# Kernel tuning notes

Measured on AMD Instinct MI355X. Metric: run time of the kernel, lower is better.

Reference implementation:

```python
import jax, jax.numpy as jnp
import numpy as np

B, N, DX, DZ, L = 512, 32, 78, 64, 1000

def _gcn_norm(A):
    # PyG gcn_norm: add remaining self loops (fill 1), symmetric D^-1/2 (A+I) D^-1/2
    n = A.shape[-1]
    A_hat = jnp.maximum(A, jnp.eye(n, dtype=A.dtype))
    dinv = jax.lax.rsqrt(A_hat.sum(-1))
    return A_hat * dinv[..., :, None] * dinv[..., None, :]

def _bn(h, g, b, eps=1e-5):
    # BatchNorm1d, training-mode batch statistics (torch default module state)
    m = jnp.mean(h, 0)
    v = jnp.var(h, 0)
    return (h - m) * jax.lax.rsqrt(v + eps) * g + b

def _conv(h, W, b):  # h [B,C,L], W [O,I,K], valid padding + ReLU (Conv1dReLU)
    y = jax.lax.conv_general_dilated(h, W, (1,), 'VALID', dimension_numbers=('NCH', 'OIH', 'NCH'))
    return jax.nn.relu(y + b[None, :, None])

def _attn(v):  # Attention.project is only Tanh in the source
    return jax.nn.softmax(jnp.tanh(v), axis=1) * v

def _forward(x, adj, target, z, dec_W0, dec_b0, dec_g0, dec_be0, dec_W1, dec_b1, dec_g1, dec_be1,
             gW1, gb1, gW2, gb2, gW3, gb3, fcg1_W, fcg1_b, fcg2_W, fcg2_b, emb,
             c10_W, c10_b, c20_W, c20_b, c21_W, c21_b, c30_W, c30_b, c31_W, c31_b, c32_W, c32_b,
             prot_W, prot_b, fc1_W, fc1_b, fc2_W, fc2_b, out_W, out_b):
    Bn = B * N
    # frozen conditional VAE decoder -> augmented features (detached)
    zc = jnp.concatenate([z.reshape(Bn, DZ), x.reshape(Bn, DX)], axis=-1)
    h = jax.nn.relu(_bn(zc @ dec_W0 + dec_b0, dec_g0, dec_be0))
    aug = jnp.tanh(_bn(h @ dec_W1 + dec_b1, dec_g1, dec_be1))
    aug = jax.lax.stop_gradient(aug).reshape(B, N, DX)
    X = jnp.concatenate([aug, x], axis=-1)  # [B,N,156]
    # 1-hop / 2-hop / 3-hop adjacency patterns (spspmm -> binary power patterns)
    A1 = _gcn_norm(adj)
    A2p = (adj @ adj > 0).astype(adj.dtype)
    A3p = (A2p @ adj > 0).astype(adj.dtype)
    A2 = _gcn_norm(A2p)
    A3 = _gcn_norm(A3p)
    gcn = lambda A, hh, W, b: jax.nn.relu(A @ (hh @ W) + b)
    h1 = gcn(A1, X, gW1, gb1)
    h2 = gcn(A1, h1, gW2, gb2)
    h3 = gcn(A1, h2, gW3, gb3)
    h5 = gcn(A2, gcn(A2, X, gW1, gb1), gW2, gb2)
    h6 = gcn(A3, X, gW1, gb1)
    hg = jnp.max(jnp.concatenate([h3, h5, h6], axis=-1), axis=1)  # gmp -> [B,1092]
    xg = jax.nn.relu(hg @ fcg1_W + fcg1_b) @ fcg2_W + fcg2_b  # dropout = identity (eval)
    xg = _attn(xg)
    # protein branch
    e = jnp.transpose(emb[target], (0, 2, 1))  # [B,128,1000]
    f1 = jnp.max(_conv(e, c10_W, c10_b), axis=-1)
    f2 = jnp.max(_conv(_conv(e, c20_W, c20_b), c21_W, c21_b), axis=-1)
    f3 = jnp.max(_conv(_conv(_conv(e, c30_W, c30_b), c31_W, c31_b), c32_W, c32_b), axis=-1)
    xt = _attn(jnp.concatenate([f1, f2, f3], axis=-1) @ prot_W + prot_b)
    xc = jnp.concatenate([xg, xt], axis=-1)
    xc = jax.nn.relu(xc @ fc1_W + fc1_b)
    xc = jax.nn.relu(xc @ fc2_W + fc2_b)
    return xc @ out_W + out_b

def setup_inputs():
    key = jax.random.key(0)
    ks = iter(jax.random.split(key, 64))
    def w(shape, s=0.05):
        return jax.random.normal(next(ks), shape, dtype=jnp.float32) * s
    x = jax.random.normal(next(ks), (B, N, DX), dtype=jnp.float32)
    r = jax.random.uniform(next(ks), (B, N, N))
    up = jnp.triu((r < 0.08).astype(jnp.float32), 1)
    adj = up + jnp.swapaxes(up, 1, 2)  # symmetric, no self loops, avg degree ~5
    target = jax.random.randint(next(ks), (B, L), 0, 26, dtype=jnp.int32)
    z = jax.random.normal(next(ks), (B, N, DZ), dtype=jnp.float32)
    emb = w((26, 128), 1.0).at[0].set(0.0)  # padding_idx=0
    return dict(x=x, adj=adj, target=target, z=z,
        dec_W0=w((DZ + DX, 256)), dec_b0=jnp.zeros(256), dec_g0=jnp.ones(256), dec_be0=jnp.zeros(256),
        dec_W1=w((256, DX)), dec_b1=jnp.zeros(DX), dec_g1=jnp.ones(DX), dec_be1=jnp.zeros(DX),
        gW1=w((156, 156)), gb1=jnp.zeros(156), gW2=w((156, 312)), gb2=jnp.zeros(312),
        gW3=w((312, 624)), gb3=jnp.zeros(624),
        fcg1_W=w((1092, 1024)), fcg1_b=jnp.zeros(1024), fcg2_W=w((1024, 128)), fcg2_b=jnp.zeros(128),
        emb=emb,
        c10_W=w((96, 128, 3)), c10_b=jnp.zeros(96),
        c20_W=w((96, 128, 3)), c20_b=jnp.zeros(96), c21_W=w((96, 96, 3)), c21_b=jnp.zeros(96),
        c30_W=w((96, 128, 3)), c30_b=jnp.zeros(96), c31_W=w((96, 96, 3)), c31_b=jnp.zeros(96),
        c32_W=w((96, 96, 3)), c32_b=jnp.zeros(96),
        prot_W=w((288, 128)), prot_b=jnp.zeros(128),
        fc1_W=w((256, 1024)), fc1_b=jnp.zeros(1024), fc2_W=w((1024, 512)), fc2_b=jnp.zeros(512),
        out_W=w((512, 1)), out_b=jnp.zeros(1))

def reference(x, adj, target, z, dec_W0, dec_b0, dec_g0, dec_be0, dec_W1, dec_b1, dec_g1, dec_be1,
              gW1, gb1, gW2, gb2, gW3, gb3, fcg1_W, fcg1_b, fcg2_W, fcg2_b, emb,
              c10_W, c10_b, c20_W, c20_b, c21_W, c21_b, c30_W, c30_b, c31_W, c31_b, c32_W, c32_b,
              prot_W, prot_b, fc1_W, fc1_b, fc2_W, fc2_b, out_W, out_b):
    return _forward(x, adj, target, z, dec_W0, dec_b0, dec_g0, dec_be0, dec_W1, dec_b1, dec_g1, dec_be1,
                    gW1, gb1, gW2, gb2, gW3, gb3, fcg1_W, fcg1_b, fcg2_W, fcg2_b, emb,
                    c10_W, c10_b, c20_W, c20_b, c21_W, c21_b, c30_W, c30_b, c31_W, c31_b, c32_W, c32_b,
                    prot_W, prot_b, fc1_W, fc1_b, fc2_W, fc2_b, out_W, out_b)
```

## Files before the change

### kernel.cpp

```cpp
#include <hip/hip_runtime.h>

static constexpr size_t O_H0    = 0;
static constexpr size_t O_H1P   = 4194304;
static constexpr size_t O_X     = 5473216;
static constexpr size_t O_A1    = 8029120;
static constexpr size_t O_A2    = 8553408;
static constexpr size_t O_A3    = 9077696;
static constexpr size_t O_H4    = 9601984;
static constexpr size_t O_H6    = 12157888;
static constexpr size_t O_H1W2  = 14713792;
static constexpr size_t O_H2    = 19825600;
static constexpr size_t O_H2W3  = 24937408;
static constexpr size_t O_H3    = 35161024;
static constexpr size_t O_HG    = 45384640;
static constexpr size_t O_FCG1O = 45943744;
static constexpr size_t O_M     = 46468032;
static constexpr size_t O_F     = 46535424;
static constexpr size_t O_V     = 46682880;
static constexpr size_t O_XC    = 46748416;
static constexpr size_t O_FC1O  = 46879488;
static constexpr size_t O_FC2O  = 47403776;
static constexpr size_t O_PART  = 47665920;
static constexpr size_t O_MV    = 47698688;
static constexpr size_t O_BT21  = 47699712;
static constexpr size_t O_BT31  = 47727360;
static constexpr size_t O_W32T  = 47755008;
static constexpr size_t O_XW1  = O_H0;
static constexpr size_t O_SK   = O_H0;
static constexpr size_t O_H1   = O_X;
static constexpr size_t O_H4W2 = O_H1W2;
static constexpr size_t O_H5   = O_H2W3;
static constexpr size_t O_R10  = O_H1W2;
static constexpr size_t O_R20  = O_H1W2 + 1687296;
static constexpr size_t O_R30  = O_H1W2 + 3374592;
static constexpr size_t O_N21  = O_H2W3;
static constexpr size_t O_N31  = O_H2W3 + 5061888;

template<int AMODE, int ACT>
__global__ __launch_bounds__(256) void gemm_k(
    const float* __restrict__ A, const float* __restrict__ Bm,
    const float* __restrict__ bias, float* __restrict__ C,
    int M, int N, int K, const float* __restrict__ A2)
{
  __shared__ __align__(16) float sA[16 * 68];
  __shared__ __align__(16) float sB[16 * 68];
  const int tid = threadIdx.x;
  const int m0 = blockIdx.y * 64, n0 = blockIdx.x * 64;
  const int tx = tid & 15, ty = tid >> 4;
  float acc[4][4] = {};
  for (int k0 = 0; k0 < K; k0 += 16) {
#pragma unroll
    for (int s2 = 0; s2 < 4; s2++) {
      int idx = tid + s2 * 256;
      int am = idx >> 4, ak = idx & 15;
      int gm = m0 + am, gk = k0 + ak;
      float va = 0.f;
      if (gm < M && gk < K) {
        if (AMODE == 0) va = A[(size_t)gm * K + gk];
        else            va = (gk < 64) ? A[gm * 64 + gk] : A2[gm * 78 + gk - 64];
      }
      sA[ak * 68 + am] = va;
      int bk2 = idx >> 6, bn = idx & 63;
      int gk2 = k0 + bk2, gn = n0 + bn;
      float vb = 0.f;
      if (gk2 < K && gn < N) vb = Bm[(size_t)gk2 * N + gn];
      sB[bk2 * 68 + bn] = vb;
    }
    __syncthreads();
#pragma unroll
    for (int kk = 0; kk < 16; kk++) {
      const float4 a4 = *(const float4*)&sA[kk * 68 + ty * 4];
      const float4 b4 = *(const float4*)&sB[kk * 68 + tx * 4];
      const float ra[4] = {a4.x, a4.y, a4.z, a4.w};
      const float rb[4] = {b4.x, b4.y, b4.z, b4.w};
#pragma unroll
      for (int i2 = 0; i2 < 4; i2++)
#pragma unroll
        for (int j2 = 0; j2 < 4; j2++)
          acc[i2][j2] = fmaf(ra[i2], rb[j2], acc[i2][j2]);
    }
    __syncthreads();
  }
#pragma unroll
  for (int i2 = 0; i2 < 4; i2++) {
    int gm = m0 + ty * 4 + i2;
    if (gm >= M) continue;
#pragma unroll
    for (int j2 = 0; j2 < 4; j2++) {
      int gn = n0 + tx * 4 + j2;
      if (gn >= N) continue;
      float v = acc[i2][j2];
      if (bias) v += bias[gn];
      if (ACT == 1) v = fmaxf(v, 0.f);
      C[(size_t)gm * N + gn] = v;
    }
  }
}

__global__ __launch_bounds__(256) void gemm_sk(
    const float* __restrict__ A, const float* __restrict__ Bm,
    float* __restrict__ PT, int M, int N, int K, int KS)
{
  __shared__ __align__(16) float sA[16 * 68];
  __shared__ __align__(16) float sB[16 * 68];
  const int tid = threadIdx.x;
  const int m0 = blockIdx.y * 64, n0 = blockIdx.x * 64;
  const int kb = blockIdx.z * KS;
  const int ke = min(K, kb + KS);
  const int tx = tid & 15, ty = tid >> 4;
  float acc[4][4] = {};
  for (int k0 = kb; k0 < ke; k0 += 16) {
#pragma unroll
    for (int s2 = 0; s2 < 4; s2++) {
      int idx = tid + s2 * 256;
      int am = idx >> 4, ak = idx & 15;
      int gm = m0 + am, gk = k0 + ak;
      float va = 0.f;
      if (gm < M && gk < ke) va = A[(size_t)gm * K + gk];
      sA[ak * 68 + am] = va;
      int bk2 = idx >> 6, bn = idx & 63;
      int gk2 = k0 + bk2, gn = n0 + bn;
      float vb = 0.f;
      if (gk2 < ke && gn < N) vb = Bm[(size_t)gk2 * N + gn];
      sB[bk2 * 68 + bn] = vb;
    }
    __syncthreads();
#pragma unroll
    for (int kk = 0; kk < 16; kk++) {
      const float4 a4 = *(const float4*)&sA[kk * 68 + ty * 4];
      const float4 b4 = *(const float4*)&sB[kk * 68 + tx * 4];
      const float ra[4] = {a4.x, a4.y, a4.z, a4.w};
      const float rb[4] = {b4.x, b4.y, b4.z, b4.w};
#pragma unroll
      for (int i2 = 0; i2 < 4; i2++)
#pragma unroll
        for (int j2 = 0; j2 < 4; j2++)
          acc[i2][j2] = fmaf(ra[i2], rb[j2], acc[i2][j2]);
    }
    __syncthreads();
  }
  float* P = PT + (size_t)blockIdx.z * M * N;
#pragma unroll
  for (int i2 = 0; i2 < 4; i2++) {
    int gm = m0 + ty * 4 + i2;
    if (gm >= M) continue;
#pragma unroll
    for (int j2 = 0; j2 < 4; j2++) {
      int gn = n0 + tx * 4 + j2;
      if (gn >= N) continue;
      P[(size_t)gm * N + gn] = acc[i2][j2];
    }
  }
}

__global__ void skred_kernel(const float* __restrict__ PT, const float* __restrict__ bias,
                             float* __restrict__ C, int MN, int nmask, int S, int act)
{
  int i = blockIdx.x * 256 + threadIdx.x;
  if (i >= MN) return;
  float s = 0.f;
  for (int z = 0; z < S; z++) s += PT[(size_t)z * MN + i];
  if (bias) s += bias[i & nmask];
  if (act) s = fmaxf(s, 0.f);
  C[i] = s;
}

template<int AMODE, int ACT>
__global__ __launch_bounds__(256) void gemm2_k(
    const float* __restrict__ A, const float* __restrict__ Bm,
    const float* __restrict__ bias, float* __restrict__ C,
    int M, int N, int K, const float* __restrict__ A2)
{
  __shared__ __align__(16) float sA[16 * 132];
  __shared__ __align__(16) float sB[16 * 68];
  const int tid = threadIdx.x;
  const int m0 = blockIdx.y * 128, n0 = blockIdx.x * 64;
  const int tx = tid & 15, ty = tid >> 4;
  float acc[8][4] = {};
  for (int k0 = 0; k0 < K; k0 += 16) {
#pragma unroll
    for (int s2 = 0; s2 < 2; s2++) {
      int idx = tid + s2 * 256;
      int am = idx >> 2, kq = idx & 3;
      int gm = m0 + am;
#pragma unroll
      for (int j = 0; j < 4; j++) {
        int gk = k0 + kq * 4 + j;
        float va = 0.f;
        if (gm < M && gk < K) {
          if (AMODE == 0) va = A[(size_t)gm * K + gk];
          else            va = (gk < 64) ? A[gm * 64 + gk] : A2[gm * 78 + gk - 64];
        }
        sA[(kq * 4 + j) * 132 + am] = va;
      }
    }
    {
      int bk = tid >> 4, bn4 = tid & 15;
      int gk2 = k0 + bk;
#pragma unroll
      for (int j = 0; j < 4; j++) {
        int gn = n0 + bn4 * 4 + j;
        float vb = 0.f;
        if (gk2 < K && gn < N) vb = Bm[(size_t)gk2 * N + gn];
        sB[bk * 68 + bn4 * 4 + j] = vb;
      }
    }
    __syncthreads();
#pragma unroll
    for (int kk = 0; kk < 16; kk++) {
      const float4 a0 = *(const float4*)&sA[kk * 132 + ty * 8];
      const float4 a1 = *(const float4*)&sA[kk * 132 + ty * 8 + 4];
      const float4 b4 = *(const float4*)&sB[kk * 68 + tx * 4];
      const float ra[8] = {a0.x, a0.y, a0.z, a0.w, a1.x, a1.y, a1.z, a1.w};
      const float rb[4] = {b4.x, b4.y, b4.z, b4.w};
#pragma unroll
      for (int i2 = 0; i2 < 8; i2++)
#pragma unroll
        for (int j2 = 0; j2 < 4; j2++)
          acc[i2][j2] = fmaf(ra[i2], rb[j2], acc[i2][j2]);
    }
    __syncthreads();
  }
#pragma unroll
  for (int i2 = 0; i2 < 8; i2++) {
    int gm = m0 + ty * 8 + i2;
    if (gm >= M) continue;
#pragma unroll
    for (int j2 = 0; j2 < 4; j2++) {
      int gn = n0 + tx * 4 + j2;
      if (gn >= N) continue;
      float v = acc[i2][j2];
      if (bias) v += bias[gn];
      if (ACT == 1) v = fmaxf(v, 0.f);
      C[(size_t)gm * N + gn] = v;
    }
  }
}

template<int AMODE, int ACT>
__global__ __launch_bounds__(256) void gemm3_k(
    const float* __restrict__ A, const float* __restrict__ Bm,
    const float* __restrict__ bias, float* __restrict__ C,
    int M, int N, int K, const float* __restrict__ A2)
{
  __shared__ __align__(16) float sA[16][132];
  __shared__ __align__(16) float sB[16][132];
  const int tid = threadIdx.x;
  const int m0 = blockIdx.y * 128, n0 = blockIdx.x * 128;
  const int tx = tid & 15, ty = tid >> 4;
  float acc[8][8] = {};
  for (int k0 = 0; k0 < K; k0 += 16) {
    {
      int am = tid >> 1;
      int kq = (tid & 1) * 8;
      int gm = m0 + am;
#pragma unroll
      for (int j = 0; j < 8; j++) {
        int gk = k0 + kq + j;
        float va = 0.f;
        if (gm < M && gk < K) {
          if (AMODE == 0) va = A[(size_t)gm * K + gk];
          else            va = (gk < 64) ? A[gm * 64 + gk] : A2[gm * 78 + gk - 64];
        }
        sA[kq + j][am] = va;
      }
      int bk = tid >> 4;
      int bn = (tid & 15) * 8;
      int gk2 = k0 + bk;
#pragma unroll
      for (int j = 0; j < 8; j++) {
        int gn = n0 + bn + j;
        float vb = 0.f;
        if (gk2 < K && gn < N) vb = Bm[(size_t)gk2 * N + gn];
        sB[bk][bn + j] = vb;
      }
    }
    __syncthreads();
#pragma unroll
    for (int kk = 0; kk < 16; kk++) {
      const float4 a0 = *(const float4*)&sA[kk][ty * 4];
      const float4 a1 = *(const float4*)&sA[kk][64 + ty * 4];
      const float4 b0 = *(const float4*)&sB[kk][tx * 4];
      const float4 b1 = *(const float4*)&sB[kk][64 + tx * 4];
      const float ra[8] = {a0.x, a0.y, a0.z, a0.w, a1.x, a1.y, a1.z, a1.w};
      const float rb[8] = {b0.x, b0.y, b0.z, b0.w, b1.x, b1.y, b1.z, b1.w};
#pragma unroll
      for (int i = 0; i < 8; i++)
#pragma unroll
        for (int j = 0; j < 8; j++)
          acc[i][j] = fmaf(ra[i], rb[j], acc[i][j]);
    }
    __syncthreads();
  }
#pragma unroll
  for (int i = 0; i < 8; i++) {
    int gm = m0 + (i < 4 ? ty * 4 + i : 64 + ty * 4 + (i - 4));
    if (gm >= M) continue;
#pragma unroll
    for (int j = 0; j < 8; j++) {
      int gn = n0 + (j < 4 ? tx * 4 + j : 64 + tx * 4 + (j - 4));
      if (gn >= N) continue;
      float v = acc[i][j];
      if (bias) v += bias[gn];
      if (ACT == 1) v = fmaxf(v, 0.f);
      C[(size_t)gm * N + gn] = v;
    }
  }
}

__global__ __launch_bounds__(256) void bn_partial(const float* __restrict__ H,
    float* __restrict__ PS, float* __restrict__ PQ, int C)
{
  int c = blockIdx.x * 64 + (threadIdx.x & 63);
  int rg = threadIdx.x >> 6;
  __shared__ float sS[256], sQ[256];
  float s = 0.f, q = 0.f;
  if (c < C) {
    int base = blockIdx.y * 256 + rg;
    for (int t = 0; t < 64; t++) {
      float v = H[(size_t)(base + 4 * t) * C + c];
      s += v; q += v * v;
    }
  }
  sS[threadIdx.x] = s; sQ[threadIdx.x] = q;
  __syncthreads();
  if (threadIdx.x < 64 && c < C) {
    float ts = sS[threadIdx.x] + sS[threadIdx.x + 64] + sS[threadIdx.x + 128] + sS[threadIdx.x + 192];
    float tq = sQ[threadIdx.x] + sQ[threadIdx.x + 64] + sQ[threadIdx.x + 128] + sQ[threadIdx.x + 192];
    PS[blockIdx.y * C + c] = ts;
    PQ[blockIdx.y * C + c] = tq;
  }
}

__global__ void bn_final(const float* __restrict__ PS, const float* __restrict__ PQ,
                         float* __restrict__ MV, int C)
{
  int c = threadIdx.x;
  if (c >= C) return;
  float s = 0.f, q = 0.f;
  for (int y = 0; y < 64; y++) { s += PS[y * C + c]; q += PQ[y * C + c]; }
  float mean = s * (1.f / 16384.f);
  float var = q * (1.f / 16384.f) - mean * mean;
  MV[c] = mean; MV[256 + c] = var;
}

__global__ void bn_norm(const float* __restrict__ IN, float* __restrict__ OUT,
                        const float* __restrict__ MV, const float* __restrict__ g,
                        const float* __restrict__ bb, int C, int ostride, int total, int act,
                        const float* __restrict__ xsrc)
{
  int idx = blockIdx.x * 256 + threadIdx.x;
  if (idx >= total) return;
  int r = idx / C, c = idx - r * C;
  float v = (IN[idx] - MV[c]) * (1.f / sqrtf(MV[256 + c] + 1e-5f)) * g[c] + bb[c];
  v = (act == 1) ? fmaxf(v, 0.f) : tanhf(v);
  OUT[(size_t)r * ostride + c] = v;
  if (xsrc) OUT[(size_t)r * ostride + 78 + c] = xsrc[idx];
}

__global__ __launch_bounds__(1024) void adj_kernel(const float* __restrict__ adj,
    float* __restrict__ A1o, float* __restrict__ A2o, float* __restrict__ A3o)
{
  int b = blockIdx.x, t = threadIdx.x;
  int i = t >> 5, j = t & 31;
  __shared__ float sA[32][33], sP[32][33];
  __shared__ float sd1[32], sd2[32], sd3[32];
  float a = adj[b * 1024 + t];
  sA[i][j] = a;
  float ah = (i == j) ? fmaxf(a, 1.f) : a;
  float rs = ah;
#pragma unroll
  for (int m = 16; m >= 1; m >>= 1) rs += __shfl_xor(rs, m, 32);
  float di = 1.f / sqrtf(rs);
  if (j == 0) sd1[i] = di;
  __syncthreads();
  A1o[b * 1024 + t] = ah * di * sd1[j];
  float c2 = 0.f;
#pragma unroll
  for (int k = 0; k < 32; k++) c2 += sA[i][k] * sA[k][j];
  float p2 = (c2 > 0.f) ? 1.f : 0.f;
  sP[i][j] = p2;
  float ah2 = (i == j) ? 1.f : p2;
  float rs2 = ah2;
#pragma unroll
  for (int m = 16; m >= 1; m >>= 1) rs2 += __shfl_xor(rs2, m, 32);
  float di2 = 1.f / sqrtf(rs2);
  if (j == 0) sd2[i] = di2;
  __syncthreads();
  A2o[b * 1024 + t] = ah2 * di2 * sd2[j];
  float c3 = 0.f;
#pragma unroll
  for (int k = 0; k < 32; k++) c3 += sP[i][k] * sA[k][j];
  float p3 = (c3 > 0.f) ? 1.f : 0.f;
  float ah3 = (i == j) ? 1.f : p3;
  float rs3 = ah3;
#pragma unroll
  for (int m = 16; m >= 1; m >>= 1) rs3 += __shfl_xor(rs3, m, 32);
  float di3 = 1.f / sqrtf(rs3);
  if (j == 0) sd3[i] = di3;
  __syncthreads();
  A3o[b * 1024 + t] = ah3 * di3 * sd3[j];
}

__global__ __launch_bounds__(64) void agg_kernel(const float* __restrict__ A,
    const float* __restrict__ HW, const float* __restrict__ bias,
    float* __restrict__ OUT, int C)
{
  int b = blockIdx.y;
  int c = blockIdx.x * 64 + threadIdx.x;
  __shared__ float sAd[1024];
  for (int e = threadIdx.x; e < 1024; e += 64) sAd[e] = A[b * 1024 + e];
  __syncthreads();
  if (c >= C) return;
  float hw[32];
  const float* hp = HW + (size_t)b * 32 * C + c;
#pragma unroll
  for (int m = 0; m < 32; m++) hw[m] = hp[(size_t)m * C];
  float bv = bias[c];
#pragma unroll 2
  for (int n = 0; n < 32; n++) {
    float s = bv;
#pragma unroll
    for (int m = 0; m < 32; m++) s = fmaf(sAd[n * 32 + m], hw[m], s);
    OUT[(size_t)b * 32 * C + (size_t)n * C + c] = fmaxf(s, 0.f);
  }
}

__global__ void hg_kernel(const float* __restrict__ h3, const float* __restrict__ h5,
                          const float* __restrict__ h6, float* __restrict__ HG)
{
  int b = blockIdx.y;
  int c = blockIdx.x * 256 + threadIdx.x;
  if (c >= 1092) return;
  const float* p; int stride;
  if (c < 624)      { p = h3 + (size_t)b * 32 * 624 + c;          stride = 624; }
  else if (c < 936) { p = h5 + (size_t)b * 32 * 312 + (c - 624);  stride = 312; }
  else              { p = h6 + (size_t)b * 32 * 156 + (c - 936);  stride = 156; }
  float m = p[0];
#pragma unroll 4
  for (int n = 1; n < 32; n++) m = fmaxf(m, p[(size_t)n * stride]);
  HG[b * 1092 + c] = m;
}

__global__ __launch_bounds__(64) void attn_kernel(const float* __restrict__ V,
    float* __restrict__ OUT, int ostride, int ooff)
{
  int r = blockIdx.x, lane = threadIdx.x;
  float v0 = V[r * 128 + lane], v1 = V[r * 128 + 64 + lane];
  float e0 = expf(tanhf(v0)), e1 = expf(tanhf(v1));
  float s = e0 + e1;
#pragma unroll
  for (int m = 32; m >= 1; m >>= 1) s += __shfl_xor(s, m);
  float inv = 1.f / s;
  OUT[r * ostride + ooff + lane] = e0 * inv * v0;
  OUT[r * ostride + ooff + 64 + lane] = e1 * inv * v1;
}

__global__ void mtable_kernel(const float* __restrict__ emb, const float* __restrict__ W10,
    const float* __restrict__ W20, const float* __restrict__ W30, float* __restrict__ M)
{
  int idx = blockIdx.x * 256 + threadIdx.x;
  if (idx >= 3 * 3 * 26 * 96) return;
  int o = idx % 96, tok = (idx / 96) % 26, k = (idx / (96 * 26)) % 3, cv = idx / (96 * 26 * 3);
  const float* W = (cv == 0) ? W10 : ((cv == 1) ? W20 : W30);
  float s = 0.f;
#pragma unroll 4
  for (int i = 0; i < 128; i++) s = fmaf(emb[tok * 128 + i], W[(o * 128 + i) * 3 + k], s);
  M[idx] = s;
}

__global__ void rtable_kernel(const float* __restrict__ M,
    const float* __restrict__ b1, const float* __restrict__ b2, const float* __restrict__ b3,
    float* __restrict__ R1, float* __restrict__ R2, float* __restrict__ R3)
{
  int cv = blockIdx.y;
  int idx = blockIdx.x * 256 + threadIdx.x;
  if (idx >= 17576 * 96) return;
  int o = idx % 96, g = idx / 96;
  int t0 = g / 676, t1 = (g / 26) % 26, t2 = g % 26;
  const float* Mc = M + cv * 3 * 26 * 96;
  float v = ((cv == 0) ? b1 : ((cv == 1) ? b2 : b3))[o];
  v += Mc[(0 * 26 + t0) * 96 + o] + Mc[(1 * 26 + t1) * 96 + o] + Mc[(2 * 26 + t2) * 96 + o];
  float* R = (cv == 0) ? R1 : ((cv == 1) ? R2 : R3);
  R[idx] = fmaxf(v, 0.f);
}

__global__ void wtrans3_kernel(const float* __restrict__ W21, const float* __restrict__ W31,
                               const float* __restrict__ W32,
                               float* __restrict__ O21, float* __restrict__ O31,
                               float* __restrict__ O32)
{
  int e = blockIdx.x * 256 + threadIdx.x;
  if (e >= 96 * 96 * 3) return;
  int job = blockIdx.y;
  const float* W = (job == 0) ? W21 : ((job == 1) ? W31 : W32);
  float* out = (job == 0) ? O21 : ((job == 1) ? O31 : O32);
  int o, i, k;
  if (job < 2) { i = e / 288; int r = e % 288; k = r / 96; o = r % 96; }
  else         { k = e / (96 * 96); i = (e / 96) % 96; o = e % 96; }
  out[e] = W[(o * 96 + i) * 3 + k];
}

__global__ __launch_bounds__(384) void conv3_fused(const int* __restrict__ target,
    const float* __restrict__ R10,
    const float* __restrict__ N21, const float* __restrict__ b21,
    const float* __restrict__ N31, const float* __restrict__ b31,
    const float* __restrict__ W32t, const float* __restrict__ b32, float* __restrict__ F)
{
  int b = blockIdx.y, tile = blockIdx.x;
  int l0 = tile * 64;
  int tid = threadIdx.x;
  __shared__ float sIn[96 * 67];
  __shared__ int sG[68];
  __shared__ unsigned sR[192];
  int ncols = min(66, 996 - l0);
  int n1    = min(66, 998 - l0);
  int nouts = min(64, 994 - l0);
  int ng    = min(68, 998 - l0);
  if (tid < 192) sR[tid] = 0u;
  for (int p = tid; p < ng; p += 384) {
    int t0 = target[b * 1000 + l0 + p];
    int t1 = target[b * 1000 + l0 + p + 1];
    int t2 = target[b * 1000 + l0 + p + 2];
    sG[p] = (t0 * 26 + t1) * 26 + t2;
  }
  __syncthreads();
  {
    int ig = tid % 24;
    int coff = tid / 24;
    int i4 = ig * 4;
    float4 v1m = make_float4(0.f, 0.f, 0.f, 0.f);
    float4 v2m = make_float4(0.f, 0.f, 0.f, 0.f);
    const float4 bb31 = *(const float4*)&b31[i4];
    const float4 bb21 = *(const float4*)&b21[i4];
    for (int c = coff; c < n1; c += 16) {
      float4 r1 = *(const float4*)&R10[(size_t)sG[c] * 96 + i4];
      v1m.x = fmaxf(v1m.x, r1.x); v1m.y = fmaxf(v1m.y, r1.y);
      v1m.z = fmaxf(v1m.z, r1.z); v1m.w = fmaxf(v1m.w, r1.w);
      if (c < ncols) {
        size_t r0 = (size_t)sG[c] * 3 + 0;
        size_t r1i = (size_t)sG[c + 1] * 3 + 1;
        size_t r2 = (size_t)sG[c + 2] * 3 + 2;
        float4 a0 = *(const float4*)&N31[r0 * 96 + i4];
        float4 a1 = *(const float4*)&N31[r1i * 96 + i4];
        float4 a2 = *(const float4*)&N31[r2 * 96 + i4];
        sIn[(i4 + 0) * 67 + c] = fmaxf(bb31.x + a0.x + a1.x + a2.x, 0.f);
        sIn[(i4 + 1) * 67 + c] = fmaxf(bb31.y + a0.y + a1.y + a2.y, 0.f);
        sIn[(i4 + 2) * 67 + c] = fmaxf(bb31.z + a0.z + a1.z + a2.z, 0.f);
        sIn[(i4 + 3) * 67 + c] = fmaxf(bb31.w + a0.w + a1.w + a2.w, 0.f);
        float4 c0 = *(const float4*)&N21[r0 * 96 + i4];
        float4 c1 = *(const float4*)&N21[r1i * 96 + i4];
        float4 c2 = *(const float4*)&N21[r2 * 96 + i4];
        v2m.x = fmaxf(v2m.x, bb21.x + c0.x + c1.x + c2.x);
        v2m.y = fmaxf(v2m.y, bb21.y + c0.y + c1.y + c2.y);
        v2m.z = fmaxf(v2m.z, bb21.z + c0.z + c1.z + c2.z);
        v2m.w = fmaxf(v2m.w, bb21.w + c0.w + c1.w + c2.w);
      }
    }
    atomicMax(&sR[i4 + 0], __float_as_uint(v1m.x));
    atomicMax(&sR[i4 + 1], __float_as_uint(v1m.y));
    atomicMax(&sR[i4 + 2], __float_as_uint(v1m.z));
    atomicMax(&sR[i4 + 3], __float_as_uint(v1m.w));
    atomicMax(&sR[96 + i4 + 0], __float_as_uint(fmaxf(v2m.x, 0.f)));
    atomicMax(&sR[96 + i4 + 1], __float_as_uint(fmaxf(v2m.y, 0.f)));
    atomicMax(&sR[96 + i4 + 2], __float_as_uint(fmaxf(v2m.z, 0.f)));
    atomicMax(&sR[96 + i4 + 3], __float_as_uint(fmaxf(v2m.w, 0.f)));
  }
  __syncthreads();
  if (tid < 192) {
    int which = tid / 96, i = tid % 96;
    atomicMax((unsigned int*)&F[b * 288 + which * 96 + i], sR[tid]);
  }
  int wv = __builtin_amdgcn_readfirstlane(tid >> 6);
  int lane = tid & 63;
  int obase = wv * 16;
  float acc[16];
#pragma unroll
  for (int jj = 0; jj < 16; jj++) acc[jj] = b32[obase + jj];
#pragma unroll 1
  for (int k = 0; k < 3; k++) {
#pragma unroll 4
    for (int i = 0; i < 96; i++) {
      float xv = sIn[i * 67 + lane + k];
      const float* wp = W32t + ((size_t)(k * 96 + i)) * 96 + obase;
#pragma unroll
      for (int jj = 0; jj < 16; jj++) acc[jj] = fmaf(xv, wp[jj], acc[jj]);
    }
  }
  bool lok = lane < nouts;
#pragma unroll
  for (int jj = 0; jj < 16; jj++) {
    float v = lok ? fmaxf(acc[jj], 0.f) : 0.f;
#pragma unroll
    for (int m = 32; m >= 1; m >>= 1) v = fmaxf(v, __shfl_xor(v, m));
    if (lane == 0) atomicMax((unsigned int*)&F[b * 288 + 192 + obase + jj], __float_as_uint(v));
  }
}

__global__ __launch_bounds__(256) void outdot_kernel(const float* __restrict__ X,
    const float* __restrict__ W, const float* __restrict__ bptr, float* __restrict__ out)
{
  int r = blockIdx.x * 4 + (threadIdx.x >> 6);
  int lane = threadIdx.x & 63;
  float s = 0.f;
  for (int j = lane; j < 512; j += 64) s = fmaf(X[(size_t)r * 512 + j], W[j], s);
#pragma unroll
  for (int m = 32; m >= 1; m >>= 1) s += __shfl_xor(s, m);
  if (lane == 0) out[r] = s + bptr[0];
}

static inline void gemm(hipStream_t st, int AMODE, int ACT,
                        const float* A, const float* B, const float* bias, float* C,
                        int M, int N, int K, const float* A2 = nullptr)
{
  dim3 g((N + 63) / 64, (M + 63) / 64), blk(256);
  if (AMODE == 0 && ACT == 0)      gemm_k<0, 0><<<g, blk, 0, st>>>(A, B, bias, C, M, N, K, A2);
  else if (AMODE == 0 && ACT == 1) gemm_k<0, 1><<<g, blk, 0, st>>>(A, B, bias, C, M, N, K, A2);
  else                             gemm_k<1, 0><<<g, blk, 0, st>>>(A, B, bias, C, M, N, K, A2);
}

static inline void gemm2(hipStream_t st, int AMODE, int ACT,
                         const float* A, const float* B, const float* bias, float* C,
                         int M, int N, int K, const float* A2 = nullptr)
{
  dim3 g((N + 63) / 64, (M + 127) / 128), blk(256);
  if (AMODE == 0 && ACT == 0)      gemm2_k<0, 0><<<g, blk, 0, st>>>(A, B, bias, C, M, N, K, A2);
  else if (AMODE == 0 && ACT == 1) gemm2_k<0, 1><<<g, blk, 0, st>>>(A, B, bias, C, M, N, K, A2);
  else                             gemm2_k<1, 0><<<g, blk, 0, st>>>(A, B, bias, C, M, N, K, A2);
}

static inline void gemm3(hipStream_t st, int AMODE, int ACT,
                         const float* A, const float* B, const float* bias, float* C,
                         int M, int N, int K, const float* A2 = nullptr)
{
  dim3 g((N + 127) / 128, (M + 127) / 128), blk(256);
  if (AMODE == 0 && ACT == 0)      gemm3_k<0, 0><<<g, blk, 0, st>>>(A, B, bias, C, M, N, K, A2);
  else if (AMODE == 0 && ACT == 1) gemm3_k<0, 1><<<g, blk, 0, st>>>(A, B, bias, C, M, N, K, A2);
  else                             gemm3_k<1, 0><<<g, blk, 0, st>>>(A, B, bias, C, M, N, K, A2);
}

static inline void gemm_splitk(hipStream_t st, const float* A, const float* B,
                               const float* bias, float* C, int M, int N, int K,
                               int S, int act, float* PT)
{
  int KS = (K + S - 1) / S;
  dim3 g((N + 63) / 64, (M + 63) / 64, S);
  gemm_sk<<<g, 256, 0, st>>>(A, B, PT, M, N, K, KS);
  int MN = M * N;
  skred_kernel<<<(MN + 255) / 256, 256, 0, st>>>(PT, bias, C, MN, N - 1, S, act);
}

extern "C" void kernel_launch(void* const* d_in, const int* in_sizes, int n_in,
                              void* d_out, int out_size, void* d_ws, size_t ws_size,
                              hipStream_t stream)
{
  (void)in_sizes; (void)n_in; (void)out_size; (void)ws_size;
  const float* x      = (const float*)d_in[0];
  const float* adj    = (const float*)d_in[1];
  const int*   target = (const int*)  d_in[2];
  const float* z      = (const float*)d_in[3];
  const float* dec_W0 = (const float*)d_in[4];
  const float* dec_b0 = (const float*)d_in[5];
  const float* dec_g0 = (const float*)d_in[6];
  const float* dec_be0= (const float*)d_in[7];
  const float* dec_W1 = (const float*)d_in[8];
  const float* dec_b1 = (const float*)d_in[9];
  const float* dec_g1 = (const float*)d_in[10];
  const float* dec_be1= (const float*)d_in[11];
  const float* gW1    = (const float*)d_in[12];
  const float* gb1    = (const float*)d_in[13];
  const float* gW2    = (const float*)d_in[14];
  const float* gb2    = (const float*)d_in[15];
  const float* gW3    = (const float*)d_in[16];
  const float* gb3    = (const float*)d_in[17];
  const float* fcg1_W = (const float*)d_in[18];
  const float* fcg1_b = (const float*)d_in[19];
  const float* fcg2_W = (const float*)d_in[20];
  const float* fcg2_b = (const float*)d_in[21];
  const float* emb    = (const float*)d_in[22];
  const float* c10_W  = (const float*)d_in[23];
  const float* c10_b  = (const float*)d_in[24];
  const float* c20_W  = (const float*)d_in[25];
  const float* c20_b  = (const float*)d_in[26];
  const float* c21_W  = (const float*)d_in[27];
  const float* c21_b  = (const float*)d_in[28];
  const float* c30_W  = (const float*)d_in[29];
  const float* c30_b  = (const float*)d_in[30];
  const float* c31_W  = (const float*)d_in[31];
  const float* c31_b  = (const float*)d_in[32];
  const float* c32_W  = (const float*)d_in[33];
  const float* c32_b  = (const float*)d_in[34];
  const float* prot_W = (const float*)d_in[35];
  const float* prot_b = (const float*)d_in[36];
  const float* fc1_W  = (const float*)d_in[37];
  const float* fc1_b  = (const float*)d_in[38];
  const float* fc2_W  = (const float*)d_in[39];
  const float* fc2_b  = (const float*)d_in[40];
  const float* out_W  = (const float*)d_in[41];
  const float* out_b  = (const float*)d_in[42];
  float* out = (float*)d_out;
  float* ws = (float*)d_ws;

  float* H0   = ws + O_H0;   float* H1P  = ws + O_H1P;  float* X    = ws + O_X;
  float* A1   = ws + O_A1;   float* A2   = ws + O_A2;   float* A3   = ws + O_A3;
  float* XW1  = ws + O_XW1;  float* H1   = ws + O_H1;   float* H4   = ws + O_H4;
  float* H6   = ws + O_H6;   float* H1W2 = ws + O_H1W2; float* H2   = ws + O_H2;
  float* H2W3 = ws + O_H2W3; float* H3   = ws + O_H3;   float* H4W2 = ws + O_H4W2;
  float* H5   = ws + O_H5;   float* HG   = ws + O_HG;   float* FCG1O= ws + O_FCG1O;
  float* Mt   = ws + O_M;    float* F    = ws + O_F;    float* V    = ws + O_V;
  float* XC   = ws + O_XC;   float* FC1O = ws + O_FC1O; float* FC2O = ws + O_FC2O;
  float* PS   = ws + O_PART; float* PQ   = ws + O_PART + 16384;
  float* MV   = ws + O_MV;   float* SK   = ws + O_SK;
  float* R10  = ws + O_R10;  float* R20  = ws + O_R20;  float* R30  = ws + O_R30;
  float* N21  = ws + O_N21;  float* N31  = ws + O_N31;
  float* BT21 = ws + O_BT21; float* BT31 = ws + O_BT31; float* W32T = ws + O_W32T;

  gemm2(stream, 1, 0, z, dec_W0, dec_b0, H0, 16384, 256, 142, x);
  bn_partial<<<dim3(4, 64), 256, 0, stream>>>(H0, PS, PQ, 256);
  bn_final<<<1, 256, 0, stream>>>(PS, PQ, MV, 256);
  bn_norm<<<16384, 256, 0, stream>>>(H0, H0, MV, dec_g0, dec_be0, 256, 256, 16384 * 256, 1, nullptr);
  gemm2(stream, 0, 0, H0, dec_W1, dec_b1, H1P, 16384, 78, 256);
  bn_partial<<<dim3(2, 64), 256, 0, stream>>>(H1P, PS, PQ, 78);
  bn_final<<<1, 256, 0, stream>>>(PS, PQ, MV, 78);
  bn_norm<<<4995, 256, 0, stream>>>(H1P, X, MV, dec_g1, dec_be1, 78, 156, 16384 * 78, 2, x);

  adj_kernel<<<512, 1024, 0, stream>>>(adj, A1, A2, A3);

  gemm2(stream, 0, 0, X, gW1, nullptr, XW1, 16384, 156, 156);
  agg_kernel<<<dim3(3, 512), 64, 0, stream>>>(A1, XW1, gb1, H1, 156);
  agg_kernel<<<dim3(3, 512), 64, 0, stream>>>(A2, XW1, gb1, H4, 156);
  agg_kernel<<<dim3(3, 512), 64, 0, stream>>>(A3, XW1, gb1, H6, 156);
  gemm3(stream, 0, 0, H1, gW2, nullptr, H1W2, 16384, 312, 156);
  agg_kernel<<<dim3(5, 512), 64, 0, stream>>>(A1, H1W2, gb2, H2, 312);
  gemm3(stream, 0, 0, H2, gW3, nullptr, H2W3, 16384, 624, 312);
  agg_kernel<<<dim3(10, 512), 64, 0, stream>>>(A1, H2W3, gb3, H3, 624);
  gemm3(stream, 0, 0, H4, gW2, nullptr, H4W2, 16384, 312, 156);
  agg_kernel<<<dim3(5, 512), 64, 0, stream>>>(A2, H4W2, gb2, H5, 312);
  hg_kernel<<<dim3(5, 512), 256, 0, stream>>>(H3, H5, H6, HG);

  gemm_splitk(stream, HG, fcg1_W, fcg1_b, FCG1O, 512, 1024, 1092, 4, 1, SK);
  gemm_splitk(stream, FCG1O, fcg2_W, fcg2_b, V, 512, 128, 1024, 8, 0, SK);
  attn_kernel<<<512, 64, 0, stream>>>(V, XC, 256, 0);

  hipMemsetAsync(F, 0, 512 * 288 * sizeof(float), stream);
  mtable_kernel<<<264, 256, 0, stream>>>(emb, c10_W, c20_W, c30_W, Mt);
  rtable_kernel<<<dim3(6591, 3), 256, 0, stream>>>(Mt, c10_b, c20_b, c30_b, R10, R20, R30);
  wtrans3_kernel<<<dim3(108, 3), 256, 0, stream>>>(c21_W, c31_W, c32_W, BT21, BT31, W32T);
  gemm3(stream, 0, 0, R20, BT21, nullptr, N21, 17576, 288, 96);
  gemm3(stream, 0, 0, R30, BT31, nullptr, N31, 17576, 288, 96);
  conv3_fused<<<dim3(16, 512), 384, 0, stream>>>(target, R10, N21, c21_b, N31, c31_b, W32T, c32_b, F);
  gemm_splitk(stream, F, prot_W, prot_b, V, 512, 128, 288, 4, 0, SK);
  attn_kernel<<<512, 64, 0, stream>>>(V, XC, 256, 128);

  gemm_splitk(stream, XC, fc1_W, fc1_b, FC1O, 512, 1024, 256, 2, 1, SK);
  gemm_splitk(stream, FC1O, fc2_W, fc2_b, FC2O, 512, 512, 1024, 4, 1, SK);
  outdot_kernel<<<128, 256, 0, stream>>>(FC2O, out_W, out_b, out);
}
```

Measured before the change: 1.376 ms.

## Pipeline conv3 gather with FMA in quarters and merge three agg launches

The fused conv3 kernel now splits the 96 input channels into four quarters. Each wave gathers the next quarter's table rows while it runs FMAs on the current quarter, so global gather latency overlaps with compute. The per-wave max reductions now use shuffles instead of a strided loop. Separately, the three first-layer aggregation launches are merged into one launch that uses a z grid dimension. This adds extra block barriers and register pressure from the prefetched float4 values.

```diff
diff --git a/kernel.cpp b/kernel.cpp
--- a/kernel.cpp
+++ b/kernel.cpp
@@ -426,6 +426,33 @@
   }
 }
 
+__global__ __launch_bounds__(64) void agg3_kernel(const float* __restrict__ A1,
+    const float* __restrict__ A2, const float* __restrict__ A3,
+    const float* __restrict__ HW, const float* __restrict__ bias,
+    float* __restrict__ O1, float* __restrict__ O2, float* __restrict__ O3, int C)
+{
+  int b = blockIdx.y;
+  int c = blockIdx.x * 64 + threadIdx.x;
+  const float* A = (blockIdx.z == 0) ? A1 : ((blockIdx.z == 1) ? A2 : A3);
+  float* OUT = (blockIdx.z == 0) ? O1 : ((blockIdx.z == 1) ? O2 : O3);
+  __shared__ float sAd[1024];
+  for (int e = threadIdx.x; e < 1024; e += 64) sAd[e] = A[b * 1024 + e];
+  __syncthreads();
+  if (c >= C) return;
+  float hw[32];
+  const float* hp = HW + (size_t)b * 32 * C + c;
+#pragma unroll
+  for (int m = 0; m < 32; m++) hw[m] = hp[(size_t)m * C];
+  float bv = bias[c];
+#pragma unroll 2
+  for (int n = 0; n < 32; n++) {
+    float s = bv;
+#pragma unroll
+    for (int m = 0; m < 32; m++) s = fmaf(sAd[n * 32 + m], hw[m], s);
+    OUT[(size_t)b * 32 * C + (size_t)n * C + c] = fmaxf(s, 0.f);
+  }
+}
+
 __global__ void hg_kernel(const float* __restrict__ h3, const float* __restrict__ h5,
                           const float* __restrict__ h6, float* __restrict__ HG)
 {
@@ -507,16 +534,16 @@
     const float* __restrict__ N31, const float* __restrict__ b31,
     const float* __restrict__ W32t, const float* __restrict__ b32, float* __restrict__ F)
 {
-  int b = blockIdx.y, tile = blockIdx.x;
-  int l0 = tile * 64;
-  int tid = threadIdx.x;
+  const int b = blockIdx.y, tile = blockIdx.x;
+  const int l0 = tile * 64;
+  const int tid = threadIdx.x;
   __shared__ float sIn[96 * 67];
   __shared__ int sG[68];
   __shared__ unsigned sR[192];
-  int ncols = min(66, 996 - l0);
-  int n1    = min(66, 998 - l0);
-  int nouts = min(64, 994 - l0);
-  int ng    = min(68, 998 - l0);
+  const int ncols = min(66, 996 - l0);
+  const int n1    = min(66, 998 - l0);
+  const int nouts = min(64, 994 - l0);
+  const int ng    = min(68, 998 - l0);
   if (tid < 192) sR[tid] = 0u;
   for (int p = tid; p < ng; p += 384) {
     int t0 = target[b * 1000 + l0 + p];
@@ -525,69 +552,130 @@
     sG[p] = (t0 * 26 + t1) * 26 + t2;
   }
   __syncthreads();
-  {
-    int ig = tid % 24;
-    int coff = tid / 24;
-    int i4 = ig * 4;
-    float4 v1m = make_float4(0.f, 0.f, 0.f, 0.f);
-    float4 v2m = make_float4(0.f, 0.f, 0.f, 0.f);
-    const float4 bb31 = *(const float4*)&b31[i4];
-    const float4 bb21 = *(const float4*)&b21[i4];
-    for (int c = coff; c < n1; c += 16) {
-      float4 r1 = *(const float4*)&R10[(size_t)sG[c] * 96 + i4];
-      v1m.x = fmaxf(v1m.x, r1.x); v1m.y = fmaxf(v1m.y, r1.y);
-      v1m.z = fmaxf(v1m.z, r1.z); v1m.w = fmaxf(v1m.w, r1.w);
+  const int wv = tid >> 6, lane = tid & 63;
+  const int obase = __builtin_amdgcn_readfirstlane(wv) * 16;
+  float acc[16];
+#pragma unroll
+  for (int jj = 0; jj < 16; jj++) acc[jj] = b32[obase + jj];
+
+  float4 r1a, a0a, a1a, a2a, c0a, c1a, c2a;
+  int g0 = 0, g1 = 0, g2 = 0;
+
+#define ISSUE(q) { \
+    const int i4 = (q) * 24 + wv * 4; \
+    if (lane < n1) g0 = sG[lane]; \
+    if (lane < ncols) { \
+      g1 = sG[lane + 1]; g2 = sG[lane + 2]; \
+      a0a = *(const float4*)&N31[((size_t)g0 * 3 + 0) * 96 + i4]; \
+      a1a = *(const float4*)&N31[((size_t)g1 * 3 + 1) * 96 + i4]; \
+      a2a = *(const float4*)&N31[((size_t)g2 * 3 + 2) * 96 + i4]; \
+      c0a = *(const float4*)&N21[((size_t)g0 * 3 + 0) * 96 + i4]; \
+      c1a = *(const float4*)&N21[((size_t)g1 * 3 + 1) * 96 + i4]; \
+      c2a = *(const float4*)&N21[((size_t)g2 * 3 + 2) * 96 + i4]; \
+    } \
+    if (lane < n1) r1a = *(const float4*)&R10[(size_t)g0 * 96 + i4]; \
+  }
+
+#define CONSUME(q) { \
+    const int i4 = (q) * 24 + wv * 4; \
+    const float4 bb31 = *(const float4*)&b31[i4]; \
+    const float4 bb21 = *(const float4*)&b21[i4]; \
+    float v1x = 0.f, v1y = 0.f, v1z = 0.f, v1w = 0.f; \
+    float v2x = 0.f, v2y = 0.f, v2z = 0.f, v2w = 0.f; \
+    if (lane < ncols) { \
+      sIn[(i4 + 0) * 67 + lane] = fmaxf(bb31.x + a0a.x + a1a.x + a2a.x, 0.f); \
+      sIn[(i4 + 1) * 67 + lane] = fmaxf(bb31.y + a0a.y + a1a.y + a2a.y, 0.f); \
+      sIn[(i4 + 2) * 67 + lane] = fmaxf(bb31.z + a0a.z + a1a.z + a2a.z, 0.f); \
+      sIn[(i4 + 3) * 67 + lane] = fmaxf(bb31.w + a0a.w + a1a.w + a2a.w, 0.f); \
+      v2x = bb21.x + c0a.x + c1a.x + c2a.x; \
+      v2y = bb21.y + c0a.y + c1a.y + c2a.y; \
+      v2z = bb21.z + c0a.z + c1a.z + c2a.z; \
+      v2w = bb21.w + c0a.w + c1a.w + c2a.w; \
+    } \
+    if (lane < n1) { v1x = r1a.x; v1y = r1a.y; v1z = r1a.z; v1w = r1a.w; } \
+    _Pragma("unroll") \
+    for (int m = 32; m >= 1; m >>= 1) { \
+      v1x = fmaxf(v1x, __shfl_xor(v1x, m)); v1y = fmaxf(v1y, __shfl_xor(v1y, m)); \
+      v1z = fmaxf(v1z, __shfl_xor(v1z, m)); v1w = fmaxf(v1w, __shfl_xor(v1w, m)); \
+      v2x = fmaxf(v2x, __shfl_xor(v2x, m)); v2y = fmaxf(v2y, __shfl_xor(v2y, m)); \
+      v2z = fmaxf(v2z, __shfl_xor(v2z, m)); v2w = fmaxf(v2w, __shfl_xor(v2w, m)); \
+    } \
+    if (lane == 0) { \
+      atomicMax(&sR[i4 + 0], __float_as_uint(v1x)); \
+      atomicMax(&sR[i4 + 1], __float_as_uint(v1y)); \
+      atomicMax(&sR[i4 + 2], __float_as_uint(v1z)); \
+      atomicMax(&sR[i4 + 3], __float_as_uint(v1w)); \
+      atomicMax(&sR[96 + i4 + 0], __float_as_uint(fmaxf(v2x, 0.f))); \
+      atomicMax(&sR[96 + i4 + 1], __float_as_uint(fmaxf(v2y, 0.f))); \
+      atomicMax(&sR[96 + i4 + 2], __float_as_uint(fmaxf(v2z, 0.f))); \
+      atomicMax(&sR[96 + i4 + 3], __float_as_uint(fmaxf(v2w, 0.f))); \
+    } \
+  }
+
+#define FMAQ(q) { \
+    _Pragma("unroll 3") \
+    for (int k = 0; k < 3; k++) { \
+      _Pragma("unroll 4") \
+      for (int ii = 0; ii < 24; ii++) { \
+        const int i = (q) * 24 + ii; \
+        const float xv = sIn[i * 67 + lane + k]; \
+        const float* wp = W32t + ((size_t)(k * 96 + i)) * 96 + obase; \
+        _Pragma("unroll") \
+        for (int jj = 0; jj < 16; jj++) acc[jj] = fmaf(xv, wp[jj], acc[jj]); \
+      } \
+    } \
+  }
+
+  ISSUE(0);
+  if (tid < 48) {
+    const int i4 = (tid % 24) * 4;
+    const int c = 64 + tid / 24;
+    if (c < n1) {
+      const int G0 = sG[c];
+      const float4 vr = *(const float4*)&R10[(size_t)G0 * 96 + i4];
+      atomicMax(&sR[i4 + 0], __float_as_uint(vr.x));
+      atomicMax(&sR[i4 + 1], __float_as_uint(vr.y));
+      atomicMax(&sR[i4 + 2], __float_as_uint(vr.z));
+      atomicMax(&sR[i4 + 3], __float_as_uint(vr.w));
       if (c < ncols) {
-        size_t r0 = (size_t)sG[c] * 3 + 0;
-        size_t r1i = (size_t)sG[c + 1] * 3 + 1;
-        size_t r2 = (size_t)sG[c + 2] * 3 + 2;
-        float4 a0 = *(const float4*)&N31[r0 * 96 + i4];
-        float4 a1 = *(const float4*)&N31[r1i * 96 + i4];
-        float4 a2 = *(const float4*)&N31[r2 * 96 + i4];
-        sIn[(i4 + 0) * 67 + c] = fmaxf(bb31.x + a0.x + a1.x + a2.x, 0.f);
-        sIn[(i4 + 1) * 67 + c] = fmaxf(bb31.y + a0.y + a1.y + a2.y, 0.f);
-        sIn[(i4 + 2) * 67 + c] = fmaxf(bb31.z + a0.z + a1.z + a2.z, 0.f);
-        sIn[(i4 + 3) * 67 + c] = fmaxf(bb31.w + a0.w + a1.w + a2.w, 0.f);
-        float4 c0 = *(const float4*)&N21[r0 * 96 + i4];
-        float4 c1 = *(const float4*)&N21[r1i * 96 + i4];
-        float4 c2 = *(const float4*)&N21[r2 * 96 + i4];
-        v2m.x = fmaxf(v2m.x, bb21.x + c0.x + c1.x + c2.x);
-        v2m.y = fmaxf(v2m.y, bb21.y + c0.y + c1.y + c2.y);
-        v2m.z = fmaxf(v2m.z, bb21.z + c0.z + c1.z + c2.z);
-        v2m.w = fmaxf(v2m.w, bb21.w + c0.w + c1.w + c2.w);
+        const int G1 = sG[c + 1], G2 = sG[c + 2];
+        const float4 tb31 = *(const float4*)&b31[i4];
+        const float4 tb21 = *(const float4*)&b21[i4];
+        const float4 A0 = *(const float4*)&N31[((size_t)G0 * 3 + 0) * 96 + i4];
+        const float4 A1 = *(const float4*)&N31[((size_t)G1 * 3 + 1) * 96 + i4];
+        const float4 A2 = *(const float4*)&N31[((size_t)G2 * 3 + 2) * 96 + i4];
+        const float4 C0 = *(const float4*)&N21[((size_t)G0 * 3 + 0) * 96 + i4];
+        const float4 C1 = *(const float4*)&N21[((size_t)G1 * 3 + 1) * 96 + i4];
+        const float4 C2 = *(const float4*)&N21[((size_t)G2 * 3 + 2) * 96 + i4];
+        sIn[(i4 + 0) * 67 + c] = fmaxf(tb31.x + A0.x + A1.x + A2.x, 0.f);
+        sIn[(i4 + 1) * 67 + c] = fmaxf(tb31.y + A0.y + A1.y + A2.y, 0.f);
+        sIn[(i4 + 2) * 67 + c] = fmaxf(tb31.z + A0.z + A1.z + A2.z, 0.f);
+        sIn[(i4 + 3) * 67 + c] = fmaxf(tb31.w + A0.w + A1.w + A2.w, 0.f);
+        atomicMax(&sR[96 + i4 + 0], __float_as_uint(fmaxf(tb21.x + C0.x + C1.x + C2.x, 0.f)));
+        atomicMax(&sR[96 + i4 + 1], __float_as_uint(fmaxf(tb21.y + C0.y + C1.y + C2.y, 0.f)));
+        atomicMax(&sR[96 + i4 + 2], __float_as_uint(fmaxf(tb21.z + C0.z + C1.z + C2.z, 0.f)));
+        atomicMax(&sR[96 + i4 + 3], __float_as_uint(fmaxf(tb21.w + C0.w + C1.w + C2.w, 0.f)));
       }
     }
-    atomicMax(&sR[i4 + 0], __float_as_uint(v1m.x));
-    atomicMax(&sR[i4 + 1], __float_as_uint(v1m.y));
-    atomicMax(&sR[i4 + 2], __float_as_uint(v1m.z));
-    atomicMax(&sR[i4 + 3], __float_as_uint(v1m.w));
-    atomicMax(&sR[96 + i4 + 0], __float_as_uint(fmaxf(v2m.x, 0.f)));
-    atomicMax(&sR[96 + i4 + 1], __float_as_uint(fmaxf(v2m.y, 0.f)));
-    atomicMax(&sR[96 + i4 + 2], __float_as_uint(fmaxf(v2m.z, 0.f)));
-    atomicMax(&sR[96 + i4 + 3], __float_as_uint(fmaxf(v2m.w, 0.f)));
-  }
-  __syncthreads();
+  }
+  CONSUME(0);
+  __syncthreads();
+  ISSUE(1); FMAQ(0); CONSUME(1);
+  __syncthreads();
+  ISSUE(2); FMAQ(1); CONSUME(2);
+  __syncthreads();
+  ISSUE(3); FMAQ(2); CONSUME(3);
+  __syncthreads();
+  FMAQ(3);
+#undef ISSUE
+#undef CONSUME
+#undef FMAQ
+
   if (tid < 192) {
     int which = tid / 96, i = tid % 96;
     atomicMax((unsigned int*)&F[b * 288 + which * 96 + i], sR[tid]);
   }
-  int wv = __builtin_amdgcn_readfirstlane(tid >> 6);
-  int lane = tid & 63;
-  int obase = wv * 16;
-  float acc[16];
-#pragma unroll
-  for (int jj = 0; jj < 16; jj++) acc[jj] = b32[obase + jj];
-#pragma unroll 1
-  for (int k = 0; k < 3; k++) {
-#pragma unroll 4
-    for (int i = 0; i < 96; i++) {
-      float xv = sIn[i * 67 + lane + k];
-      const float* wp = W32t + ((size_t)(k * 96 + i)) * 96 + obase;
-#pragma unroll
-      for (int jj = 0; jj < 16; jj++) acc[jj] = fmaf(xv, wp[jj], acc[jj]);
-    }
-  }
-  bool lok = lane < nouts;
+  const bool lok = lane < nouts;
 #pragma unroll
   for (int jj = 0; jj < 16; jj++) {
     float v = lok ? fmaxf(acc[jj], 0.f) : 0.f;
@@ -727,9 +815,7 @@
   adj_kernel<<<512, 1024, 0, stream>>>(adj, A1, A2, A3);
 
   gemm2(stream, 0, 0, X, gW1, nullptr, XW1, 16384, 156, 156);
-  agg_kernel<<<dim3(3, 512), 64, 0, stream>>>(A1, XW1, gb1, H1, 156);
-  agg_kernel<<<dim3(3, 512), 64, 0, stream>>>(A2, XW1, gb1, H4, 156);
-  agg_kernel<<<dim3(3, 512), 64, 0, stream>>>(A3, XW1, gb1, H6, 156);
+  agg3_kernel<<<dim3(3, 512, 3), 64, 0, stream>>>(A1, A2, A3, XW1, gb1, H1, H4, H6, 156);
   gemm3(stream, 0, 0, H1, gW2, nullptr, H1W2, 16384, 312, 156);
   agg_kernel<<<dim3(5, 512), 64, 0, stream>>>(A1, H1W2, gb2, H2, 312);
   gemm3(stream, 0, 0, H2, gW3, nullptr, H2W3, 16384, 624, 312);
```

Result: slower. 1.686 ms (+22.5%).
